# Kernel tuning notes

Hardware: AMD Instinct MI355X
Metric: run time of the kernel (lower is better)

Reference implementation:

```python
import jax, jax.numpy as jnp
import numpy as np

# B videos, K topological sorts, N subtask nodes, S video segments, H = hsize
B, K, N, S, H = 8, 4, 16, 64, 512
NEG = -100.0  # torch.full((N,S), -100.0) init in dp_align


def setup_inputs() -> dict:
    key = jax.random.key(0)
    ks = jax.random.split(key, 6)
    return {
        "seg_text_feats": jax.random.normal(ks[0], (B, K, N, 2 * H), jnp.float32),
        "vid_feature": jax.random.normal(ks[1], (B, S, 2 * H), jnp.float32),
        "labels": jax.random.uniform(ks[2], (B,), jnp.float32),
        "W1": jax.random.normal(ks[3], (4 * H, H), jnp.float32) * 0.02,
        "b1": jnp.zeros((H,), jnp.float32),
        "w2": jax.random.normal(ks[4], (H,), jnp.float32) * 0.04,
        "b2": jnp.zeros((), jnp.float32),
    }


def _dp_single(logits):
    """Viterbi-style banded DP of dp_align for one (video, sort) pair.
    logits: [N, S]. Returns (best_score=arr[0,0], aggregated_logits, alignment[N]).
    Recurrence (faithful to the torch code):
      arr[n,s] = max(V_curr, arr[n,s+1]) where
        V_curr = logsig(logit[n,s])                     if n == N-1
        V_curr = logsig(logit[n,s]) + arr[n+1, s]       otherwise
      band: s in [n, S-N+n]; out-of-band cells stay -100.
    """
    n_nodes, n_segs = logits.shape
    L = jax.nn.log_sigmoid(logits)
    s_idx = jnp.arange(n_segs)

    def row_step(arr_next, xn):
        n, Ln = xn
        c = jnp.where(n == n_nodes - 1, Ln, Ln + arr_next)  # V_opt_curr per segment
        in_band = (s_idx >= n) & (s_idx <= n_segs - n_nodes + n)
        # arr[n,s] = max(max_{s'>=s in band} c[s'], -100)  (reverse cummax == seg loop)
        cm = jax.lax.cummax(jnp.where(in_band, c, -jnp.inf)[::-1])[::-1]
        row = jnp.where(in_band, jnp.maximum(cm, NEG), NEG)
        # choice[s]: took V_opt_curr (ties -> curr, matching >=); base case s=S-1 forced curr
        row_nxt = jnp.concatenate([row[1:], jnp.full((1,), -1e30, row.dtype)])
        choice = in_band & (c >= row_nxt)
        return row, (row, choice)

    arr0 = jnp.full((n_segs,), NEG, logits.dtype)
    xs = (jnp.arange(n_nodes - 1, -1, -1), L[::-1])  # nodes processed bottom-up
    _, (rows, choices) = jax.lax.scan(row_step, arr0, xs)
    best = rows[-1][0]          # arr[0, 0]
    choice = choices[::-1]      # reorder to ascending node index

    # Backpointer traceback: curr -> (node+1, seg+1) (record seg), next -> (node, seg+1)
    def step(state, _):
        node, seg, done, agg, align = state
        took = (~done) & choice[node, seg]
        agg = agg + jnp.where(took, logits[node, seg], 0.0)
        align = align.at[node].set(jnp.where(took, seg, align[node]))
        done = done | (took & (node == n_nodes - 1))
        node = jnp.where(took & (~done), node + 1, node)
        seg = jnp.where(done, seg, jnp.minimum(seg + 1, n_segs - 1))
        return (node, seg, done, agg, align), None

    init = (jnp.int32(0), jnp.int32(0), jnp.bool_(False),
            jnp.zeros((), logits.dtype), jnp.zeros((n_nodes,), jnp.int32))
    (_, _, _, agg, align), _ = jax.lax.scan(step, init, None, length=n_nodes + n_segs)
    return best, agg, align


def reference(seg_text_feats, vid_feature, labels, W1, b1, w2, b2):
    Bx, Kx, Nx, F2 = seg_text_feats.shape
    Sx = vid_feature.shape[1]
    # Batched query MLP over all (sort, node, segment) pairs (replaces the per-pair
    # batch-1 Linear+ReLU+Linear launches in the torch loop). Dropout(0.5) is eval-mode identity.
    t = jnp.broadcast_to(seg_text_feats[:, :, :, None, :], (Bx, Kx, Nx, Sx, F2))
    v = jnp.broadcast_to(vid_feature[:, None, None, :, :], (Bx, Kx, Nx, Sx, F2))
    cat = jnp.concatenate([t, v], axis=-1)                      # [B,K,N,S,4H]
    h1 = jax.nn.relu(jnp.einsum('bknsf,fh->bknsh', cat, W1) + b1)
    logits = jnp.einsum('bknsh,h->bkns', h1, w2) + b2           # [B,K,N,S]

    best, agg, align = jax.vmap(jax.vmap(_dp_single))(logits)   # [B,K], [B,K], [B,K,N]
    k = jnp.argmax(best, axis=-1)                               # best sort per video
    agg_b = jnp.take_along_axis(agg, k[:, None], axis=1)[:, 0]
    align_b = jnp.take_along_axis(align, k[:, None, None], axis=1)[:, 0]
    probs = jax.nn.sigmoid(agg_b)                               # ent_probs, [B]
    return probs, labels, align_b
```

## Files before the change

### kernel.cpp

```cpp
#include <hip/hip_runtime.h>
#include <math.h>

#define Bsz 8
#define Kc 4
#define Nn 16
#define Ss 64
#define Hh 512
#define F2 1024

__device__ __forceinline__ float logsigf(float x) {
    return fminf(x, 0.0f) - log1pf(expf(-fabsf(x)));
}

template<int Ctrl, int RowMask>
__device__ __forceinline__ float dpp_add(float x) {
    int v = __builtin_amdgcn_update_dpp(0, __float_as_int(x), Ctrl, RowMask, 0xf, false);
    return x + __int_as_float(v);
}
template<int Ctrl, int RowMask>
__device__ __forceinline__ float dpp_max(float x) {
    int v = __builtin_amdgcn_update_dpp(__float_as_int(-INFINITY), __float_as_int(x),
                                        Ctrl, RowMask, 0xf, false);
    return fmaxf(x, __int_as_float(v));
}
__device__ __forceinline__ float wave_scan_add(float x) {
    x = dpp_add<0x111, 0xf>(x); x = dpp_add<0x112, 0xf>(x);
    x = dpp_add<0x114, 0xf>(x); x = dpp_add<0x118, 0xf>(x);
    x = dpp_add<0x142, 0xa>(x); x = dpp_add<0x143, 0xc>(x);
    return x;
}
__device__ __forceinline__ float wave_scan_max(float x) {
    x = dpp_max<0x111, 0xf>(x); x = dpp_max<0x112, 0xf>(x);
    x = dpp_max<0x114, 0xf>(x); x = dpp_max<0x118, 0xf>(x);
    x = dpp_max<0x142, 0xa>(x); x = dpp_max<0x143, 0xc>(x);
    return x;
}

__global__ __launch_bounds__(512) void gemm_kernel(
    const float* __restrict__ seg, const float* __restrict__ vid,
    const float* __restrict__ W1,
    float* __restrict__ Tfin, float* __restrict__ Vfin)
{
    const int lin = blockIdx.x;
    const int xcd = lin & 7;
    const int idx = lin >> 3;
    const int z   = xcd >> 2;
    const int xx  = (xcd & 3) * 2 + (idx & 1);
    const int yy  = idx >> 1;
    const float* __restrict__ Amat = z ? vid : seg;
    const float* __restrict__ Bmat = W1 + (z ? (size_t)F2 * Hh : 0);
    float* __restrict__ Out = z ? Vfin : Tfin;
    const int r0 = xx * 64;
    const int n0 = yy * 32;

    const int t = threadIdx.x;
    const int w = t >> 6;
    const int l = t & 63;
    const int kbase = w << 7;

    __shared__ __align__(16) float smem[26624];
    float* As_w = smem + w * 2176;
    float* Bs_w = smem + 17408 + w * 1152;

    const int a_row = l >> 2;
    const int a_c   = (l & 3) << 2;
    const int b_kk  = l >> 3;
    const int b_c   = (l & 7) << 2;
    const int mt    = (l >> 3) << 3;
    const int nt    = (l & 7) << 2;

    float4 sa[4], sb[2];
    auto load_step = [&](int s) {
        const int k0 = kbase + s * 16;
        #pragma unroll
        for (int i = 0; i < 4; ++i)
            sa[i] = *reinterpret_cast<const float4*>(
                Amat + (size_t)(r0 + a_row + 16 * i) * F2 + k0 + a_c);
        #pragma unroll
        for (int i = 0; i < 2; ++i)
            sb[i] = *reinterpret_cast<const float4*>(
                Bmat + (size_t)(k0 + b_kk + 8 * i) * Hh + n0 + b_c);
    };
    auto write_step = [&](int buf) {
        #pragma unroll
        for (int i = 0; i < 4; ++i) {
            const int row = a_row + 16 * i;
            float* dst = As_w + buf * 1088;
            dst[(a_c + 0) * 68 + row] = sa[i].x;
            dst[(a_c + 1) * 68 + row] = sa[i].y;
            dst[(a_c + 2) * 68 + row] = sa[i].z;
            dst[(a_c + 3) * 68 + row] = sa[i].w;
        }
        #pragma unroll
        for (int i = 0; i < 2; ++i)
            *reinterpret_cast<float4*>(
                &Bs_w[buf * 576 + (b_kk + 8 * i) * 36 + b_c]) = sb[i];
    };

    float acc[8][4];
    #pragma unroll
    for (int i = 0; i < 8; ++i)
        #pragma unroll
        for (int j = 0; j < 4; ++j) acc[i][j] = 0.f;

    auto compute = [&](int buf) {
        #pragma unroll
        for (int kk = 0; kk < 16; ++kk) {
            const float* ar = As_w + buf * 1088 + kk * 68 + mt;
            float4 a0 = *reinterpret_cast<const float4*>(ar);
            float4 a1 = *reinterpret_cast<const float4*>(ar + 4);
            float4 b  = *reinterpret_cast<const float4*>(
                Bs_w + buf * 576 + kk * 36 + nt);
            float av[8] = {a0.x, a0.y, a0.z, a0.w, a1.x, a1.y, a1.z, a1.w};
            float bv[4] = {b.x, b.y, b.z, b.w};
            #pragma unroll
            for (int i = 0; i < 8; ++i)
                #pragma unroll
                for (int j = 0; j < 4; ++j)
                    acc[i][j] = fmaf(av[i], bv[j], acc[i][j]);
        }
    };

    load_step(0);
    write_step(0);
    load_step(1);
    #pragma unroll 1
    for (int s = 0; s < 8; ++s) {
        const int cur = s & 1;
        compute(cur);
        if (s + 1 < 8) {
            write_step(cur ^ 1);
            if (s + 2 < 8) load_step(s + 2);
        }
    }

    __syncthreads();
    float* red = smem;
    #pragma unroll
    for (int i8 = 0; i8 < 8; ++i8)
        *reinterpret_cast<float4*>(&red[w * 2304 + l * 36 + 4 * i8]) =
            make_float4(acc[i8][0], acc[i8][1], acc[i8][2], acc[i8][3]);
    __syncthreads();
    {
        const int l_orig = w * 8 + (l >> 3);
        const int off = l_orig * 36 + 4 * (l & 7);
        float4 o = make_float4(0.f, 0.f, 0.f, 0.f);
        #pragma unroll
        for (int p = 0; p < 8; ++p) {
            float4 v = *reinterpret_cast<const float4*>(&red[p * 2304 + off]);
            o.x += v.x; o.y += v.y; o.z += v.z; o.w += v.w;
        }
        const int m = w * 8 + (l & 7);
        const int n = (l >> 3) << 2;
        *reinterpret_cast<float4*>(Out + (size_t)(r0 + m) * Hh + n0 + n) = o;
    }
}

__global__ __launch_bounds__(256) void combine_kernel(
    const float* __restrict__ Tfin, const float* __restrict__ Vfin,
    const float* __restrict__ b1, const float* __restrict__ w2,
    const float* __restrict__ b2, float* __restrict__ logits)
{
    const int bid = blockIdx.x;
    const int b  = bid >> 6;
    const int sc = (bid >> 3) & 7;
    const int rq = bid & 7;
    const int t = threadIdx.x;
    const int wave = t >> 6, lane = t & 63;
    __shared__ float Vs[8][516];
    {
        const int row = t >> 5;
        const int f0  = t & 31;
        const float* src = Vfin + (size_t)(b * Ss + sc * 8 + row) * Hh;
        #pragma unroll
        for (int j = 0; j < 4; ++j)
            *reinterpret_cast<float4*>(&Vs[row][(f0 + 32 * j) * 4]) =
                *reinterpret_cast<const float4*>(src + (f0 + 32 * j) * 4);
    }
    float w2r[8], b1r[8];
    #pragma unroll
    for (int j = 0; j < 8; ++j) { w2r[j] = w2[lane + 64 * j]; b1r[j] = b1[lane + 64 * j]; }
    const float bias2 = b2[0];
    float tj0[8], tj1[8];
    {
        const int r0i = b * 64 + rq * 8 + wave * 2;
        const float* t0 = Tfin + (size_t)r0i * Hh;
        const float* t1 = t0 + Hh;
        #pragma unroll
        for (int j = 0; j < 8; ++j) {
            tj0[j] = t0[lane + 64 * j] + b1r[j];
            tj1[j] = t1[lane + 64 * j] + b1r[j];
        }
    }
    __syncthreads();
    const int rbase = b * 64 + rq * 8 + wave * 2;
    #pragma unroll
    for (int si = 0; si < 8; ++si) {
        float s0 = 0.f, s1 = 0.f;
        #pragma unroll
        for (int j = 0; j < 8; ++j) {
            const float v = Vs[si][lane + 64 * j];
            s0 = fmaf(fmaxf(tj0[j] + v, 0.f), w2r[j], s0);
            s1 = fmaf(fmaxf(tj1[j] + v, 0.f), w2r[j], s1);
        }
        s0 = wave_scan_add(s0);
        s1 = wave_scan_add(s1);
        if (lane == 63) {
            logits[(size_t)rbase * Ss + sc * 8 + si]       = s0 + bias2;
            logits[(size_t)(rbase + 1) * Ss + sc * 8 + si] = s1 + bias2;
        }
    }
}

__global__ __launch_bounds__(256) void dp_kernel(
    const float* __restrict__ logits, const float* __restrict__ labels,
    float* __restrict__ out)
{
    const int b = blockIdx.x;
    const int t = threadIdx.x;
    const int k = t >> 6, rl = t & 63;
    const int sI = 63 - rl;
    __shared__ float lgs[Kc][Nn][Ss];
    __shared__ unsigned long long ch[Kc][Nn];
    __shared__ float bestS[Kc], aggS[Kc];
    __shared__ int alS[Kc][Nn];
    const float* lg = logits + (size_t)((b * Kc + k) * Nn) * Ss;
    float lv[Nn];
    #pragma unroll
    for (int n = 0; n < Nn; ++n) {
        lv[n] = lg[n * Ss + sI];
        lgs[k][n][sI] = lv[n];
    }
    float arr = -100.0f;
    #pragma unroll
    for (int n = Nn - 1; n >= 0; --n) {
        const float L = logsigf(lv[n]);
        const float c = (n == Nn - 1) ? L : (L + arr);
        const bool in_band = (rl <= 63 - n) && (rl >= 15 - n);
        float m = in_band ? c : -INFINITY;
        m = wave_scan_max(m);
        const float row = in_band ? fmaxf(m, -100.0f) : -100.0f;
        float rnA = __int_as_float(__builtin_amdgcn_update_dpp(
            __float_as_int(-1e30f), __float_as_int(row), 0x111, 0xf, 0xf, false));
        float b15 = __int_as_float(__builtin_amdgcn_update_dpp(
            0, __float_as_int(row), 0x142, 0xa, 0xf, false));
        float b31 = __int_as_float(__builtin_amdgcn_update_dpp(
            0, __float_as_int(row), 0x143, 0xc, 0xf, false));
        float rn = ((rl & 15) == 0 && rl != 0) ? ((rl == 32) ? b31 : b15) : rnA;
        unsigned long long mask = __ballot(in_band && (c >= rn));
        if (rl == 0) ch[k][n] = __brevll(mask);
        arr = row;
    }
    const float best = __shfl(arr, 63);
    __syncthreads();
    if (rl == 0) {
        float agg = 0.f;
        int start = 0;
        bool dead = false;
        int alignv[Nn];
        #pragma unroll
        for (int n = 0; n < Nn; ++n) {
            unsigned long long m2 = dead ? 0ull : (ch[k][n] & (~0ull << start));
            if (m2) {
                const int s = __builtin_ctzll(m2);
                agg += lgs[k][n][s];
                alignv[n] = s;
                start = s + 1;
            } else {
                alignv[n] = 0;
                dead = true;
            }
        }
        bestS[k] = best; aggS[k] = agg;
        #pragma unroll
        for (int n = 0; n < Nn; ++n) alS[k][n] = alignv[n];
    }
    __syncthreads();
    if (t == 0) {
        int kb = 0; float bb = bestS[0];
        #pragma unroll
        for (int kk = 1; kk < Kc; ++kk)
            if (bestS[kk] > bb) { bb = bestS[kk]; kb = kk; }
        out[b] = 1.0f / (1.0f + expf(-aggS[kb]));
        out[Bsz + b] = labels[b];
        #pragma unroll
        for (int n = 0; n < Nn; ++n)
            out[2 * Bsz + b * Nn + n] = (float)alS[kb][n];
    }
}

extern "C" void kernel_launch(void* const* d_in, const int* in_sizes, int n_in,
                              void* d_out, int out_size, void* d_ws, size_t ws_size,
                              hipStream_t stream) {
    const float* seg    = (const float*)d_in[0];
    const float* vid    = (const float*)d_in[1];
    const float* labels = (const float*)d_in[2];
    const float* W1     = (const float*)d_in[3];
    const float* b1     = (const float*)d_in[4];
    const float* w2     = (const float*)d_in[5];
    const float* b2     = (const float*)d_in[6];
    float* out = (float*)d_out;

    float* Tfin   = (float*)d_ws;
    float* Vfin   = Tfin + (size_t)512 * Hh;
    float* logits = Vfin + (size_t)512 * Hh;

    hipLaunchKernelGGL(gemm_kernel, dim3(256), dim3(512), 0, stream,
                       seg, vid, W1, Tfin, Vfin);
    hipLaunchKernelGGL(combine_kernel, dim3(512), dim3(256), 0, stream,
                       Tfin, Vfin, b1, w2, b2, logits);
    hipLaunchKernelGGL(dp_kernel, dim3(Bsz), dim3(256), 0, stream, logits, labels, out);
}
```

Measured before the change: 52.94 us.

## Load A operand directly into registers, bypassing shared-memory staging

The GEMM kernel stops staging the A tile through LDS with a transposed scatter. Each lane now loads its own 8 rows as float4 directly from global memory into two alternating register sets, so the next k-quad is prefetched while the current one is computed. Only B still goes through double-buffered LDS, which shrinks shared memory use and removes the strided transposing LDS writes. The cost is uncoalesced per-lane global loads of A, since lanes stride by whole rows, and more live registers.

```diff
diff --git a/kernel.cpp b/kernel.cpp
--- a/kernel.cpp
+++ b/kernel.cpp
@@ -58,43 +58,40 @@
     const int l = t & 63;
     const int kbase = w << 7;
 
-    __shared__ __align__(16) float smem[26624];
-    float* As_w = smem + w * 2176;
-    float* Bs_w = smem + 17408 + w * 1152;
-
-    const int a_row = l >> 2;
-    const int a_c   = (l & 3) << 2;
-    const int b_kk  = l >> 3;
-    const int b_c   = (l & 7) << 2;
-    const int mt    = (l >> 3) << 3;
-    const int nt    = (l & 7) << 2;
-
-    float4 sa[4], sb[2];
-    auto load_step = [&](int s) {
+    __shared__ __align__(16) float smem[18432];
+    float* Bs_w = smem + w * 1152;
+
+    const int b_kk = l >> 3;
+    const int b_c  = (l & 7) << 2;
+    const int mt   = (l >> 3) << 3;
+    const int nt   = (l & 7) << 2;
+
+    const float* pR[8];
+    #pragma unroll
+    for (int i = 0; i < 8; ++i)
+        pR[i] = Amat + (size_t)(r0 + mt + i) * F2 + kbase;
+
+    float4 bA, bB;
+    auto loadB = [&](int s) {
         const int k0 = kbase + s * 16;
-        #pragma unroll
-        for (int i = 0; i < 4; ++i)
-            sa[i] = *reinterpret_cast<const float4*>(
-                Amat + (size_t)(r0 + a_row + 16 * i) * F2 + k0 + a_c);
-        #pragma unroll
-        for (int i = 0; i < 2; ++i)
-            sb[i] = *reinterpret_cast<const float4*>(
-                Bmat + (size_t)(k0 + b_kk + 8 * i) * Hh + n0 + b_c);
-    };
-    auto write_step = [&](int buf) {
-        #pragma unroll
-        for (int i = 0; i < 4; ++i) {
-            const int row = a_row + 16 * i;
-            float* dst = As_w + buf * 1088;
-            dst[(a_c + 0) * 68 + row] = sa[i].x;
-            dst[(a_c + 1) * 68 + row] = sa[i].y;
-            dst[(a_c + 2) * 68 + row] = sa[i].z;
-            dst[(a_c + 3) * 68 + row] = sa[i].w;
-        }
-        #pragma unroll
-        for (int i = 0; i < 2; ++i)
-            *reinterpret_cast<float4*>(
-                &Bs_w[buf * 576 + (b_kk + 8 * i) * 36 + b_c]) = sb[i];
+        bA = *reinterpret_cast<const float4*>(Bmat + (size_t)(k0 + b_kk) * Hh + n0 + b_c);
+        bB = *reinterpret_cast<const float4*>(Bmat + (size_t)(k0 + b_kk + 8) * Hh + n0 + b_c);
+    };
+    auto writeB = [&](int buf) {
+        *reinterpret_cast<float4*>(&Bs_w[buf * 576 + b_kk * 36 + b_c]) = bA;
+        *reinterpret_cast<float4*>(&Bs_w[buf * 576 + (b_kk + 8) * 36 + b_c]) = bB;
+    };
+
+    float4 aP[8], aQ[8];
+    auto loadA_P = [&](int q) {
+        #pragma unroll
+        for (int i = 0; i < 8; ++i)
+            aP[i] = *reinterpret_cast<const float4*>(pR[i] + q * 4);
+    };
+    auto loadA_Q = [&](int q) {
+        #pragma unroll
+        for (int i = 0; i < 8; ++i)
+            aQ[i] = *reinterpret_cast<const float4*>(pR[i] + q * 4);
     };
 
     float acc[8][4];
@@ -103,34 +100,56 @@
         #pragma unroll
         for (int j = 0; j < 4; ++j) acc[i][j] = 0.f;
 
-    auto compute = [&](int buf) {
-        #pragma unroll
-        for (int kk = 0; kk < 16; ++kk) {
-            const float* ar = As_w + buf * 1088 + kk * 68 + mt;
-            float4 a0 = *reinterpret_cast<const float4*>(ar);
-            float4 a1 = *reinterpret_cast<const float4*>(ar + 4);
-            float4 b  = *reinterpret_cast<const float4*>(
-                Bs_w + buf * 576 + kk * 36 + nt);
-            float av[8] = {a0.x, a0.y, a0.z, a0.w, a1.x, a1.y, a1.z, a1.w};
+    auto quadP = [&](int buf, int qq) {
+        #pragma unroll
+        for (int j = 0; j < 4; ++j) {
+            float4 b = *reinterpret_cast<const float4*>(
+                &Bs_w[buf * 576 + (qq * 4 + j) * 36 + nt]);
             float bv[4] = {b.x, b.y, b.z, b.w};
             #pragma unroll
-            for (int i = 0; i < 8; ++i)
+            for (int i = 0; i < 8; ++i) {
+                const float a = j == 0 ? aP[i].x : j == 1 ? aP[i].y : j == 2 ? aP[i].z : aP[i].w;
                 #pragma unroll
-                for (int j = 0; j < 4; ++j)
-                    acc[i][j] = fmaf(av[i], bv[j], acc[i][j]);
-        }
-    };
-
-    load_step(0);
-    write_step(0);
-    load_step(1);
+                for (int jj = 0; jj < 4; ++jj)
+                    acc[i][jj] = fmaf(a, bv[jj], acc[i][jj]);
+            }
+        }
+    };
+    auto quadQ = [&](int buf, int qq) {
+        #pragma unroll
+        for (int j = 0; j < 4; ++j) {
+            float4 b = *reinterpret_cast<const float4*>(
+                &Bs_w[buf * 576 + (qq * 4 + j) * 36 + nt]);
+            float bv[4] = {b.x, b.y, b.z, b.w};
+            #pragma unroll
+            for (int i = 0; i < 8; ++i) {
+                const float a = j == 0 ? aQ[i].x : j == 1 ? aQ[i].y : j == 2 ? aQ[i].z : aQ[i].w;
+                #pragma unroll
+                for (int jj = 0; jj < 4; ++jj)
+                    acc[i][jj] = fmaf(a, bv[jj], acc[i][jj]);
+            }
+        }
+    };
+
+    loadB(0); writeB(0); loadB(1);
+    loadA_P(0);
     #pragma unroll 1
     for (int s = 0; s < 8; ++s) {
         const int cur = s & 1;
-        compute(cur);
+        #pragma unroll
+        for (int qq = 0; qq < 4; ++qq) {
+            const int q = s * 4 + qq;
+            if ((qq & 1) == 0) {
+                if (q + 1 < 32) loadA_Q(q + 1);
+                quadP(cur, qq);
+            } else {
+                if (q + 1 < 32) loadA_P(q + 1);
+                quadQ(cur, qq);
+            }
+        }
         if (s + 1 < 8) {
-            write_step(cur ^ 1);
-            if (s + 2 < 8) load_step(s + 2);
+            writeB(cur ^ 1);
+            if (s + 2 < 8) loadB(s + 2);
         }
     }
 
```

After: 49.52 us. 1.07x faster.

## Halve GEMM N-tile, double grid, load A directly to registers

Applied to the files above, without the earlier changes.

The GEMM kernel now uses a 64x16 output tile per block instead of 64x32 and launches twice as many blocks. A is read straight from global memory into registers with a four-deep software pipeline rather than being transposed through shared memory. B still goes through a smaller double-buffered shared tile, and the cross-wave reduction is resized to match. The aim is more parallelism across CUs and lower LDS use and traffic, at the cost of reading A twice as often overall and uncoalesced per-thread row loads of A.

```diff
diff --git a/kernel.cpp b/kernel.cpp
--- a/kernel.cpp
+++ b/kernel.cpp
@@ -51,108 +51,105 @@
     const float* __restrict__ Bmat = W1 + (z ? (size_t)F2 * Hh : 0);
     float* __restrict__ Out = z ? Vfin : Tfin;
     const int r0 = xx * 64;
-    const int n0 = yy * 32;
+    const int n0 = yy * 16;
 
     const int t = threadIdx.x;
     const int w = t >> 6;
     const int l = t & 63;
     const int kbase = w << 7;
 
-    __shared__ __align__(16) float smem[26624];
-    float* As_w = smem + w * 2176;
-    float* Bs_w = smem + 17408 + w * 1152;
-
-    const int a_row = l >> 2;
-    const int a_c   = (l & 3) << 2;
-    const int b_kk  = l >> 3;
-    const int b_c   = (l & 7) << 2;
-    const int mt    = (l >> 3) << 3;
-    const int nt    = (l & 7) << 2;
-
-    float4 sa[4], sb[2];
-    auto load_step = [&](int s) {
-        const int k0 = kbase + s * 16;
-        #pragma unroll
-        for (int i = 0; i < 4; ++i)
-            sa[i] = *reinterpret_cast<const float4*>(
-                Amat + (size_t)(r0 + a_row + 16 * i) * F2 + k0 + a_c);
-        #pragma unroll
-        for (int i = 0; i < 2; ++i)
-            sb[i] = *reinterpret_cast<const float4*>(
-                Bmat + (size_t)(k0 + b_kk + 8 * i) * Hh + n0 + b_c);
+    __shared__ __align__(16) float smem[9216];
+    float* Bs_w = smem + w * 640;
+
+    const int b_kk = l >> 2;
+    const int b_c  = (l & 3) << 2;
+    const int mt   = (l >> 2) << 2;
+    const int nt   = (l & 3) << 2;
+
+    const float* pR[4];
+    #pragma unroll
+    for (int i = 0; i < 4; ++i)
+        pR[i] = Amat + (size_t)(r0 + mt + i) * F2 + kbase;
+
+    float4 bReg;
+    auto loadB = [&](int s) {
+        bReg = *reinterpret_cast<const float4*>(
+            Bmat + (size_t)(kbase + s * 16 + b_kk) * Hh + n0 + b_c);
     };
-    auto write_step = [&](int buf) {
-        #pragma unroll
-        for (int i = 0; i < 4; ++i) {
-            const int row = a_row + 16 * i;
-            float* dst = As_w + buf * 1088;
-            dst[(a_c + 0) * 68 + row] = sa[i].x;
-            dst[(a_c + 1) * 68 + row] = sa[i].y;
-            dst[(a_c + 2) * 68 + row] = sa[i].z;
-            dst[(a_c + 3) * 68 + row] = sa[i].w;
-        }
-        #pragma unroll
-        for (int i = 0; i < 2; ++i)
-            *reinterpret_cast<float4*>(
-                &Bs_w[buf * 576 + (b_kk + 8 * i) * 36 + b_c]) = sb[i];
+    auto writeB = [&](int buf) {
+        *reinterpret_cast<float4*>(&Bs_w[buf * 320 + b_kk * 20 + b_c]) = bReg;
     };
 
-    float acc[8][4];
-    #pragma unroll
-    for (int i = 0; i < 8; ++i)
+    float4 a0[4], a1[4], a2[4], a3[4];
+    float acc[4][4];
+    #pragma unroll
+    for (int i = 0; i < 4; ++i)
         #pragma unroll
         for (int j = 0; j < 4; ++j) acc[i][j] = 0.f;
 
-    auto compute = [&](int buf) {
-        #pragma unroll
-        for (int kk = 0; kk < 16; ++kk) {
-            const float* ar = As_w + buf * 1088 + kk * 68 + mt;
-            float4 a0 = *reinterpret_cast<const float4*>(ar);
-            float4 a1 = *reinterpret_cast<const float4*>(ar + 4);
-            float4 b  = *reinterpret_cast<const float4*>(
-                Bs_w + buf * 576 + kk * 36 + nt);
-            float av[8] = {a0.x, a0.y, a0.z, a0.w, a1.x, a1.y, a1.z, a1.w};
-            float bv[4] = {b.x, b.y, b.z, b.w};
-            #pragma unroll
-            for (int i = 0; i < 8; ++i)
-                #pragma unroll
-                for (int j = 0; j < 4; ++j)
-                    acc[i][j] = fmaf(av[i], bv[j], acc[i][j]);
-        }
-    };
-
-    load_step(0);
-    write_step(0);
-    load_step(1);
+#define LOAD_A(BUF, Q) { \
+    const int _q = (Q); \
+    _Pragma("unroll") \
+    for (int i = 0; i < 4; ++i) \
+        BUF[i] = *reinterpret_cast<const float4*>(pR[i] + _q * 4); }
+
+#define QUAD(BUF, CUR, QQ) { \
+    _Pragma("unroll") \
+    for (int j = 0; j < 4; ++j) { \
+        float4 b = *reinterpret_cast<const float4*>( \
+            &Bs_w[(CUR) * 320 + ((QQ) * 4 + j) * 20 + nt]); \
+        float bv[4] = {b.x, b.y, b.z, b.w}; \
+        _Pragma("unroll") \
+        for (int i = 0; i < 4; ++i) { \
+            const float a = j == 0 ? BUF[i].x : j == 1 ? BUF[i].y \
+                          : j == 2 ? BUF[i].z : BUF[i].w; \
+            _Pragma("unroll") \
+            for (int jj = 0; jj < 4; ++jj) \
+                acc[i][jj] = fmaf(a, bv[jj], acc[i][jj]); \
+        } } }
+
+    loadB(0); writeB(0); loadB(1);
+    LOAD_A(a0, 0);
+    LOAD_A(a1, 1);
     #pragma unroll 1
     for (int s = 0; s < 8; ++s) {
         const int cur = s & 1;
-        compute(cur);
+        const int q0 = s * 4;
+        if (q0 + 2 < 32) LOAD_A(a2, q0 + 2);
+        QUAD(a0, cur, 0);
+        if (q0 + 3 < 32) LOAD_A(a3, q0 + 3);
+        QUAD(a1, cur, 1);
+        if (q0 + 4 < 32) LOAD_A(a0, q0 + 4);
+        QUAD(a2, cur, 2);
+        if (q0 + 5 < 32) LOAD_A(a1, q0 + 5);
+        QUAD(a3, cur, 3);
         if (s + 1 < 8) {
-            write_step(cur ^ 1);
-            if (s + 2 < 8) load_step(s + 2);
-        }
-    }
+            writeB(cur ^ 1);
+            if (s + 2 < 8) loadB(s + 2);
+        }
+    }
+#undef LOAD_A
+#undef QUAD
 
     __syncthreads();
     float* red = smem;
     #pragma unroll
-    for (int i8 = 0; i8 < 8; ++i8)
-        *reinterpret_cast<float4*>(&red[w * 2304 + l * 36 + 4 * i8]) =
-            make_float4(acc[i8][0], acc[i8][1], acc[i8][2], acc[i8][3]);
+    for (int i = 0; i < 4; ++i)
+        *reinterpret_cast<float4*>(&red[w * 1152 + l * 18 + 4 * i]) =
+            make_float4(acc[i][0], acc[i][1], acc[i][2], acc[i][3]);
     __syncthreads();
     {
-        const int l_orig = w * 8 + (l >> 3);
-        const int off = l_orig * 36 + 4 * (l & 7);
-        float4 o = make_float4(0.f, 0.f, 0.f, 0.f);
+        const int m  = t >> 3;
+        const int n2 = t & 7;
+        const int lp = ((m >> 2) << 2) | (n2 >> 1);
+        const int off = lp * 18 + (m & 3) * 4 + (n2 & 1) * 2;
+        float2 o = make_float2(0.f, 0.f);
         #pragma unroll
         for (int p = 0; p < 8; ++p) {
-            float4 v = *reinterpret_cast<const float4*>(&red[p * 2304 + off]);
-            o.x += v.x; o.y += v.y; o.z += v.z; o.w += v.w;
-        }
-        const int m = w * 8 + (l & 7);
-        const int n = (l >> 3) << 2;
-        *reinterpret_cast<float4*>(Out + (size_t)(r0 + m) * Hh + n0 + n) = o;
+            float2 v = *reinterpret_cast<const float2*>(&red[p * 1152 + off]);
+            o.x += v.x; o.y += v.y;
+        }
+        *reinterpret_cast<float2*>(Out + (size_t)(r0 + m) * Hh + n0 + n2 * 2) = o;
     }
 }
 
@@ -305,7 +302,7 @@
     float* Vfin   = Tfin + (size_t)512 * Hh;
     float* logits = Vfin + (size_t)512 * Hh;
 
-    hipLaunchKernelGGL(gemm_kernel, dim3(256), dim3(512), 0, stream,
+    hipLaunchKernelGGL(gemm_kernel, dim3(512), dim3(512), 0, stream,
                        seg, vid, W1, Tfin, Vfin);
     hipLaunchKernelGGL(combine_kernel, dim3(512), dim3(256), 0, stream,
                        Tfin, Vfin, b1, w2, b2, logits);
```

Result: faster. 50.43 us (-4.7%).
